# Optimization experiments

Measured on AMD Instinct MI355X. Metric: run time of the kernel, lower is better.

Reference implementation:

```python
import jax, jax.numpy as jnp
import numpy as np

B, PS, H, W = 32, 1536, 32, 64
TNS = H * W                 # total_num_selects = 2048
NJ = TNS // 16              # num_joints = 128
QK = PS // 4                # q/k channels = 384
NC = 200                    # num_classes
BN_EPS = 1e-5


def setup_inputs() -> dict:
    key = jax.random.key(0)
    ks = jax.random.split(key, 8)
    s = 0.02  # small init scale for weights
    inp = {
        "x": jax.random.normal(ks[0], (B, PS, H, W), jnp.float32),
        # param_pool0: Linear(TNS -> NJ)
        "w_pool0": jax.random.normal(ks[1], (NJ, TNS), jnp.float32) * s,
        "b_pool0": jnp.zeros((NJ,), jnp.float32),
        # learnable adjacency: eye/100 + 1/100
        "adj1": jnp.eye(NJ, dtype=jnp.float32) / 100.0 + 1.0 / 100.0,
        # conv_q1 / conv_k1: Conv1d(PS -> PS//4, kernel=1)
        "w_q": jax.random.normal(ks[2], (QK, PS), jnp.float32) * s,
        "b_q": jnp.zeros((QK,), jnp.float32),
        "w_k": jax.random.normal(ks[3], (QK, PS), jnp.float32) * s,
        "b_k": jnp.zeros((QK,), jnp.float32),
        # alpha1 (torch inits to 0; we use 0.1 so attention branch has nonzero effect/grads)
        "alpha": jnp.array([0.1], jnp.float32),
        # conv1: Conv1d(PS -> PS, kernel=1)
        "w_c1": jax.random.normal(ks[4], (PS, PS), jnp.float32) * s,
        "b_c1": jnp.zeros((PS,), jnp.float32),
        # batch_norm1 affine params
        "gamma": jnp.ones((PS,), jnp.float32),
        "beta": jnp.zeros((PS,), jnp.float32),
        # param_pool1: Linear(NJ -> 1)
        "w_pool1": jax.random.normal(ks[5], (1, NJ), jnp.float32) * s,
        "b_pool1": jnp.zeros((1,), jnp.float32),
        # classifier: Linear(PS -> NC)
        "w_cls": jax.random.normal(ks[6], (NC, PS), jnp.float32) * s,
        "b_cls": jnp.zeros((NC,), jnp.float32),
    }
    return inp


def reference(x, w_pool0, b_pool0, adj1, w_q, b_q, w_k, b_k, alpha,
              w_c1, b_c1, gamma, beta, w_pool1, b_pool1, w_cls, b_cls):
    b, c = x.shape[0], x.shape[1]
    hs = x.reshape(b, c, -1)                                   # (B, PS, TNS)
    # param_pool0: pool selects down to joints
    hs = jnp.einsum('bcs,js->bcj', hs, w_pool0) + b_pool0      # (B, PS, NJ)
    # 1x1-conv q/k then mean over channel dim
    q1 = (jnp.einsum('oc,bcj->boj', w_q, hs) + b_q[:, None]).mean(axis=1)  # (B, NJ)
    k1 = (jnp.einsum('oc,bcj->boj', w_k, hs) + b_k[:, None]).mean(axis=1)  # (B, NJ)
    # outer-difference attention, tanh-bounded, blended with learnable adjacency
    A1 = adj1 + jnp.tanh(q1[:, :, None] - k1[:, None, :]) * alpha[0]       # (B, NJ, NJ)
    # conv1 (1x1) then adjacency-weighted matmul
    hs = jnp.einsum('oc,bcj->boj', w_c1, hs) + b_c1[:, None]   # (B, PS, NJ)
    hs = jnp.einsum('bcj,bjk->bck', hs, A1)                    # (B, PS, NJ)
    # BatchNorm1d over (batch, joints) per channel (training-mode batch stats)
    mean = hs.mean(axis=(0, 2))
    var = hs.var(axis=(0, 2))
    hs = (hs - mean[None, :, None]) * jax.lax.rsqrt(var + BN_EPS)[None, :, None]
    hs = gamma[None, :, None] * hs + beta[None, :, None]
    # param_pool1 (NJ -> 1), dropout is identity in eval, flatten, classify
    hs = jnp.einsum('bcj,j->bc', hs, w_pool1[0]) + b_pool1[0]  # (B, PS)
    out = hs @ w_cls.T + b_cls                                 # (B, NC)
    return out
```

## Files before the change

### kernel.cpp

```cpp
#include <hip/hip_runtime.h>
#include <hip/hip_bf16.h>

#define B_ 32
#define PS_ 1536
#define TNS_ 2048
#define NJ_ 128
#define QK_ 384
#define NC_ 200
#define BN_EPS_ 1e-5f

typedef __attribute__((ext_vector_type(8))) short short8;
typedef __attribute__((ext_vector_type(4))) float float4v;
typedef unsigned short ushort_t;

__device__ __forceinline__ unsigned short f2b(float f) {
    unsigned int u = __float_as_uint(f);
    return (unsigned short)((u + 0x7FFFu + ((u >> 16) & 1u)) >> 16);
}
__device__ __forceinline__ float b2f_lo(unsigned int u) { return __uint_as_float(u << 16); }
__device__ __forceinline__ float b2f_hi(unsigned int u) { return __uint_as_float(u & 0xffff0000u); }

__device__ __forceinline__ void mma_chunk42(const short* As, const short* Bs,
                                            int wm, int wn, int lane, float4v acc[4][2]) {
    const int m0 = wm + (lane & 15);
    const int n0 = wn + (lane & 15);
    const int quad = lane >> 4;
    #pragma unroll
    for (int kk = 0; kk < 64; kk += 32) {
        short8 a[4], b[2];
        const int kb = quad * 8 + kk;
        #pragma unroll
        for (int i = 0; i < 4; ++i) a[i] = *(const short8*)&As[(m0 + i * 16) * 72 + kb];
        #pragma unroll
        for (int j = 0; j < 2; ++j) b[j] = *(const short8*)&Bs[(n0 + j * 16) * 72 + kb];
        #pragma unroll
        for (int i = 0; i < 4; ++i)
            #pragma unroll
            for (int j = 0; j < 2; ++j)
                acc[i][j] = __builtin_amdgcn_mfma_f32_16x16x32_bf16(a[i], b[j], acc[i][j], 0, 0, 0);
    }
}

__device__ __forceinline__ void stage_f32_512(const float* __restrict__ src, size_t stride,
                                              short* dst, int tid) {
    #pragma unroll
    for (int p = 0; p < 4; ++p) {
        int r = (tid >> 4) + p * 32;
        int kq = (tid & 15) * 4;
        float4 v = *(const float4*)(src + (size_t)r * stride + kq);
        ushort4 u = { f2b(v.x), f2b(v.y), f2b(v.z), f2b(v.w) };
        *(ushort4*)&dst[r * 72 + kq] = u;
    }
}
__device__ __forceinline__ void stage_b16_512(const ushort_t* __restrict__ src, size_t stride,
                                              short* dst, int tid) {
    #pragma unroll
    for (int p = 0; p < 2; ++p) {
        int r = (tid >> 3) + p * 64;
        int kq = (tid & 7) * 8;
        uint4 v = *(const uint4*)(src + (size_t)r * stride + kq);
        *(uint4*)&dst[r * 72 + kq] = v;
    }
}

__global__ void k_prep_all(const float* __restrict__ wq, const float* __restrict__ bq,
                           const float* __restrict__ wk, const float* __restrict__ bk,
                           const float* __restrict__ wp1,
                           const float* __restrict__ w0, const float* __restrict__ wc1,
                           float* __restrict__ wqb, float* __restrict__ wkb,
                           float* __restrict__ scal,
                           float* __restrict__ bnsum, float* __restrict__ bnsq,
                           float* __restrict__ q1, float* __restrict__ k1,
                           ushort_t* __restrict__ w0b, ushort_t* __restrict__ wc1b) {
    const int blk = blockIdx.x;
    const int tid = threadIdx.x;
    if (blk < 6) {
        int c = blk * 256 + tid;
        float s = 0.f;
        for (int o = 0; o < QK_; ++o) s += wq[(size_t)o * PS_ + c];
        wqb[c] = s * (1.0f / QK_);
        bnsum[c] = 0.f; bnsq[c] = 0.f;
    } else if (blk < 12) {
        int c = (blk - 6) * 256 + tid;
        float s = 0.f;
        for (int o = 0; o < QK_; ++o) s += wk[(size_t)o * PS_ + c];
        wkb[c] = s * (1.0f / QK_);
    } else if (blk == 12) {
        __shared__ float red[256];
        float s = (tid < QK_ ? bq[tid] : 0.f) + (tid + 256 < QK_ ? bq[tid + 256] : 0.f);
        red[tid] = s; __syncthreads();
        for (int off = 128; off > 0; off >>= 1) { if (tid < off) red[tid] += red[tid + off]; __syncthreads(); }
        if (tid == 0) scal[0] = red[0] * (1.0f / QK_);
        __syncthreads();
        s = (tid < QK_ ? bk[tid] : 0.f) + (tid + 256 < QK_ ? bk[tid + 256] : 0.f);
        red[tid] = s; __syncthreads();
        for (int off = 128; off > 0; off >>= 1) { if (tid < off) red[tid] += red[tid + off]; __syncthreads(); }
        if (tid == 0) scal[1] = red[0] * (1.0f / QK_);
        __syncthreads();
        s = (tid < NJ_ ? wp1[tid] : 0.f);
        red[tid] = s; __syncthreads();
        for (int off = 128; off > 0; off >>= 1) { if (tid < off) red[tid] += red[tid + off]; __syncthreads(); }
        if (tid == 0) scal[2] = red[0];
    } else if (blk < 269) {
        int i = (blk - 13) * 256 + tid;
        float4 v = ((const float4*)w0)[i];
        ushort4 u = { f2b(v.x), f2b(v.y), f2b(v.z), f2b(v.w) };
        ((ushort4*)w0b)[i] = u;
    } else if (blk < 2573) {
        int i = (blk - 269) * 256 + tid;
        float4 v = ((const float4*)wc1)[i];
        ushort4 u = { f2b(v.x), f2b(v.y), f2b(v.z), f2b(v.w) };
        ((ushort4*)wc1b)[i] = u;
    } else {
        int i = (blk - 2573) * 256 + tid;
        if (i < 4096) q1[i] = 0.f; else k1[i - 4096] = 0.f;
    }
}

__global__ __launch_bounds__(512) void k_gemm1(const float* __restrict__ x,
        const ushort_t* __restrict__ w0b, const float* __restrict__ b0,
        const float* __restrict__ wqb, const float* __restrict__ wkb,
        ushort_t* __restrict__ hsT, float* __restrict__ q1, float* __restrict__ k1) {
    __shared__ __align__(16) short As[128 * 72];
    __shared__ __align__(16) short Bs[128 * 72];
    const int tid = threadIdx.x, lane = tid & 63, wave = tid >> 6;
    const int wm = (wave >> 2) * 64, wn = (wave & 3) * 32;
    const size_t m0r = (size_t)blockIdx.x * 128;
    float4v acc[4][2] = {};
    for (int k0 = 0; k0 < TNS_; k0 += 64) {
        stage_f32_512(x + m0r * TNS_ + k0, TNS_, As, tid);
        stage_b16_512(w0b + k0, TNS_, Bs, tid);
        __syncthreads();
        mma_chunk42(As, Bs, wm, wn, lane, acc);
        __syncthreads();
    }
    const int b = blockIdx.x / 12, cb = (blockIdx.x % 12) * 128;
    const int quad = lane >> 4, s = lane & 15;
    float sq[2] = { 0.f, 0.f }, sk[2] = { 0.f, 0.f };
    #pragma unroll
    for (int jn = 0; jn < 2; ++jn) {
        int j = wn + jn * 16 + s;
        float bj = b0[j];
        #pragma unroll
        for (int im = 0; im < 4; ++im) {
            int c = cb + wm + im * 16 + quad * 4;
            float4v v = acc[im][jn];
            unsigned short us[4];
            #pragma unroll
            for (int r = 0; r < 4; ++r) {
                us[r] = f2b(v[r] + bj);
                float vr = b2f_lo((unsigned int)us[r]);
                sq[jn] += wqb[c + r] * vr;
                sk[jn] += wkb[c + r] * vr;
            }
            ushort4 u = { us[0], us[1], us[2], us[3] };
            *(ushort4*)&hsT[((size_t)(b * NJ_ + j)) * PS_ + c] = u;
        }
    }
    #pragma unroll
    for (int jn = 0; jn < 2; ++jn) {
        sq[jn] += __shfl_xor(sq[jn], 16, 64); sq[jn] += __shfl_xor(sq[jn], 32, 64);
        sk[jn] += __shfl_xor(sk[jn], 16, 64); sk[jn] += __shfl_xor(sk[jn], 32, 64);
    }
    if (quad == 0) {
        #pragma unroll
        for (int jn = 0; jn < 2; ++jn) {
            int j = wn + jn * 16 + s;
            atomicAdd(&q1[b * NJ_ + j], sq[jn]);
            atomicAdd(&k1[b * NJ_ + j], sk[jn]);
        }
    }
}

__global__ void k_a1(const float* __restrict__ adj, const float* __restrict__ q1,
                     const float* __restrict__ k1, const float* __restrict__ alpha,
                     const float* __restrict__ scal, ushort_t* __restrict__ A1t) {
    int idx = blockIdx.x * 256 + threadIdx.x;
    int b = idx >> 14;
    int r = idx & 16383;
    int j2 = r >> 7;
    int j = r & 127;
    float dbias = scal[0] - scal[1];
    float t = tanhf(q1[b * NJ_ + j] - k1[b * NJ_ + j2] + dbias);
    A1t[idx] = f2b(adj[j * NJ_ + j2] + t * alpha[0]);
}

__global__ __launch_bounds__(512) void k_gemm23(const ushort_t* __restrict__ wc1b,
        const float* __restrict__ bc1, const ushort_t* __restrict__ hsT,
        const ushort_t* __restrict__ A1t, const float* __restrict__ wp1,
        float* __restrict__ bnsum, float* __restrict__ bnsq, float* __restrict__ dout) {
    __shared__ __align__(16) short sm[2][128 * 72];
    __shared__ float bns_s[NJ_], bnq_s[NJ_], ds_s[NJ_];
    const int tid = threadIdx.x, lane = tid & 63, wave = tid >> 6;
    const int wm = (wave >> 2) * 64, wn = (wave & 3) * 32;
    const int b = blockIdx.y, ob = blockIdx.x * 128;
    if (tid < NJ_) { bns_s[tid] = 0.f; bnq_s[tid] = 0.f; ds_s[tid] = 0.f; }
    float4v acc[4][2] = {};
    const ushort_t* Abase = wc1b + (size_t)ob * PS_;
    const ushort_t* Bbase = hsT + (size_t)b * NJ_ * PS_;
    for (int k0 = 0; k0 < PS_; k0 += 64) {
        stage_b16_512(Abase + k0, PS_, sm[0], tid);
        stage_b16_512(Bbase + k0, PS_, sm[1], tid);
        __syncthreads();
        mma_chunk42(sm[0], sm[1], wm, wn, lane, acc);
        __syncthreads();
    }
    short* C1 = &sm[0][0];
    const int quad = lane >> 4, s = lane & 15;
    #pragma unroll
    for (int im = 0; im < 4; ++im) {
        int o0l = wm + im * 16 + quad * 4;
        float bc[4] = { bc1[ob + o0l], bc1[ob + o0l + 1], bc1[ob + o0l + 2], bc1[ob + o0l + 3] };
        #pragma unroll
        for (int jn = 0; jn < 2; ++jn) {
            int j = wn + jn * 16 + s;
            float4v v = acc[im][jn];
            #pragma unroll
            for (int r = 0; r < 4; ++r)
                C1[(o0l + r) * 136 + j] = (short)f2b(v[r] + bc[r]);
        }
    }
    __syncthreads();
    float4v acc2[4][2] = {};
    const ushort_t* Ap = A1t + (size_t)b * NJ_ * NJ_;
    const int m0 = wm + s, n0 = wn + s;
    #pragma unroll
    for (int kk = 0; kk < 128; kk += 32) {
        short8 a[4], bf[2];
        const int kb = quad * 8 + kk;
        #pragma unroll
        for (int i = 0; i < 4; ++i) a[i] = *(const short8*)&C1[(m0 + i * 16) * 136 + kb];
        #pragma unroll
        for (int j = 0; j < 2; ++j) bf[j] = *(const short8*)&Ap[(size_t)(n0 + j * 16) * NJ_ + kb];
        #pragma unroll
        for (int i = 0; i < 4; ++i)
            #pragma unroll
            for (int j = 0; j < 2; ++j)
                acc2[i][j] = __builtin_amdgcn_mfma_f32_16x16x32_bf16(a[i], bf[j], acc2[i][j], 0, 0, 0);
    }
    #pragma unroll
    for (int im = 0; im < 4; ++im) {
        float s4[4] = {}, q4[4] = {}, d4[4] = {};
        #pragma unroll
        for (int jn = 0; jn < 2; ++jn) {
            int j2 = wn + jn * 16 + s;
            float w1 = wp1[j2];
            float4v v = acc2[im][jn];
            #pragma unroll
            for (int r = 0; r < 4; ++r) {
                float vr = b2f_lo((unsigned int)f2b(v[r]));
                s4[r] += vr; q4[r] += vr * vr; d4[r] += w1 * vr;
            }
        }
        #pragma unroll
        for (int m = 1; m < 16; m <<= 1)
            #pragma unroll
            for (int r = 0; r < 4; ++r) {
                s4[r] += __shfl_xor(s4[r], m, 64);
                q4[r] += __shfl_xor(q4[r], m, 64);
                d4[r] += __shfl_xor(d4[r], m, 64);
            }
        if (s == 0) {
            #pragma unroll
            for (int r = 0; r < 4; ++r) {
                int cl = wm + im * 16 + quad * 4 + r;
                atomicAdd(&bns_s[cl], s4[r]);
                atomicAdd(&bnq_s[cl], q4[r]);
                atomicAdd(&ds_s[cl], d4[r]);
            }
        }
    }
    __syncthreads();
    if (tid < NJ_) {
        atomicAdd(&bnsum[ob + tid], bns_s[tid]);
        atomicAdd(&bnsq[ob + tid], bnq_s[tid]);
        dout[(size_t)b * PS_ + ob + tid] = ds_s[tid];
    }
}

__global__ void k_cls(const float* __restrict__ dout, const float* __restrict__ bnsum,
                      const float* __restrict__ bnsq, const float* __restrict__ gamma,
                      const float* __restrict__ beta, const float* __restrict__ scal,
                      const float* __restrict__ bp1, const float* __restrict__ wcls,
                      const float* __restrict__ bcls, float* __restrict__ out) {
    int gid = blockIdx.x * 256 + threadIdx.x;
    int w = gid >> 6;
    int lane = gid & 63;
    int b = w / 200, n = w % 200;
    const float* dp = dout + (size_t)b * PS_;
    const float* wp = wcls + (size_t)n * PS_;
    float sc2 = scal[2], bb = bp1[0];
    float acc = 0.f;
    for (int c = lane; c < PS_; c += 64) {
        float mean = bnsum[c] * (1.0f / 4096.0f);
        float var = bnsq[c] * (1.0f / 4096.0f) - mean * mean;
        float sc = gamma[c] * rsqrtf(var + BN_EPS_);
        float pval = sc * dp[c] + (beta[c] - sc * mean) * sc2 + bb;
        acc += wp[c] * pval;
    }
    #pragma unroll
    for (int off = 32; off > 0; off >>= 1) acc += __shfl_down(acc, off, 64);
    if (lane == 0) out[w] = acc + bcls[n];
}

extern "C" void kernel_launch(void* const* d_in, const int* in_sizes, int n_in,
                              void* d_out, int out_size, void* d_ws, size_t ws_size,
                              hipStream_t stream) {
    const float* x       = (const float*)d_in[0];
    const float* w_pool0 = (const float*)d_in[1];
    const float* b_pool0 = (const float*)d_in[2];
    const float* adj1    = (const float*)d_in[3];
    const float* w_q     = (const float*)d_in[4];
    const float* b_q     = (const float*)d_in[5];
    const float* w_k     = (const float*)d_in[6];
    const float* b_k     = (const float*)d_in[7];
    const float* alpha   = (const float*)d_in[8];
    const float* w_c1    = (const float*)d_in[9];
    const float* b_c1    = (const float*)d_in[10];
    const float* gamma   = (const float*)d_in[11];
    const float* beta    = (const float*)d_in[12];
    const float* w_pool1 = (const float*)d_in[13];
    const float* b_pool1 = (const float*)d_in[14];
    const float* w_cls   = (const float*)d_in[15];
    const float* b_cls   = (const float*)d_in[16];
    float* out = (float*)d_out;

    ushort_t* hsT  = (ushort_t*)d_ws;
    ushort_t* hs2  = hsT + 6291456;
    ushort_t* hs3b = hs2 + 6291456;
    ushort_t* w0b  = hs3b + 6291456;
    ushort_t* wc1b = w0b + 262144;
    ushort_t* A1t  = wc1b + 2359296;
    float* fb    = (float*)(A1t + 524288);
    float* wqb   = fb;
    float* wkb   = wqb + 1536;
    float* scal  = wkb + 1536;
    float* q1    = scal + 16;
    float* k1    = q1 + 4096;
    float* bnsum = k1 + 4096;
    float* bnsq  = bnsum + 1536;
    float* dbuf  = bnsq + 1536;
    size_t need = 44040192u + (size_t)(1536 + 1536 + 16 + 4096 + 4096 + 1536 + 1536 + 49152) * 4;
    if (ws_size < need) return;

    k_prep_all<<<2605, 256, 0, stream>>>(w_q, b_q, w_k, b_k, w_pool1, w_pool0, w_c1,
                                         wqb, wkb, scal, bnsum, bnsq, q1, k1, w0b, wc1b);
    k_gemm1 <<<384, 512, 0, stream>>>(x, w0b, b_pool0, wqb, wkb, hsT, q1, k1);
    k_a1    <<<2048, 256, 0, stream>>>(adj1, q1, k1, alpha, scal, A1t);
    k_gemm23<<<dim3(12, 32), 512, 0, stream>>>(wc1b, b_c1, hsT, A1t, w_pool1,
                                               bnsum, bnsq, dbuf);
    k_cls   <<<1600, 256, 0, stream>>>(dbuf, bnsum, bnsq, gamma, beta, scal,
                                       b_pool1, w_cls, b_cls, out);
}
```

Measured before the change: 667.8 us.

## Halve GEMM block tiles to 64 rows and swizzle gemm23 block order

Both MFMA GEMM kernels move from 128x128 tiles with 512 threads to 64x128 tiles with 256 threads. This doubles the grid to 768 blocks so the 256 CUs are better filled than with 384 blocks. k_gemm23 also flattens its grid and swizzles block indices so that blocks sharing the same batch's hsT slice are spread across the eight interleave groups. The cost is that each B tile is reloaded twice as often, and the per-block BN and dout reductions now cover 64 channels instead of 128.

```diff
diff --git a/kernel.cpp b/kernel.cpp
--- a/kernel.cpp
+++ b/kernel.cpp
@@ -21,8 +21,8 @@
 __device__ __forceinline__ float b2f_hi(unsigned int u) { return __uint_as_float(u & 0xffff0000u); }
 
 __device__ __forceinline__ void mma_chunk42(const short* As, const short* Bs,
-                                            int wm, int wn, int lane, float4v acc[4][2]) {
-    const int m0 = wm + (lane & 15);
+                                            int wn, int lane, float4v acc[4][2]) {
+    const int m0 = lane & 15;
     const int n0 = wn + (lane & 15);
     const int quad = lane >> 4;
     #pragma unroll
@@ -41,22 +41,32 @@
     }
 }
 
-__device__ __forceinline__ void stage_f32_512(const float* __restrict__ src, size_t stride,
+__device__ __forceinline__ void stage_f32_64r(const float* __restrict__ src, size_t stride,
                                               short* dst, int tid) {
     #pragma unroll
     for (int p = 0; p < 4; ++p) {
-        int r = (tid >> 4) + p * 32;
+        int r = (tid >> 4) + p * 16;
         int kq = (tid & 15) * 4;
         float4 v = *(const float4*)(src + (size_t)r * stride + kq);
         ushort4 u = { f2b(v.x), f2b(v.y), f2b(v.z), f2b(v.w) };
         *(ushort4*)&dst[r * 72 + kq] = u;
     }
 }
-__device__ __forceinline__ void stage_b16_512(const ushort_t* __restrict__ src, size_t stride,
+__device__ __forceinline__ void stage_b16_128r(const ushort_t* __restrict__ src, size_t stride,
+                                               short* dst, int tid) {
+    #pragma unroll
+    for (int p = 0; p < 4; ++p) {
+        int r = (tid >> 3) + p * 32;
+        int kq = (tid & 7) * 8;
+        uint4 v = *(const uint4*)(src + (size_t)r * stride + kq);
+        *(uint4*)&dst[r * 72 + kq] = v;
+    }
+}
+__device__ __forceinline__ void stage_b16_64r(const ushort_t* __restrict__ src, size_t stride,
                                               short* dst, int tid) {
     #pragma unroll
     for (int p = 0; p < 2; ++p) {
-        int r = (tid >> 3) + p * 64;
+        int r = (tid >> 3) + p * 32;
         int kq = (tid & 7) * 8;
         uint4 v = *(const uint4*)(src + (size_t)r * stride + kq);
         *(uint4*)&dst[r * 72 + kq] = v;
@@ -117,24 +127,25 @@
     }
 }
 
-__global__ __launch_bounds__(512) void k_gemm1(const float* __restrict__ x,
+__global__ __launch_bounds__(256) void k_gemm1(const float* __restrict__ x,
         const ushort_t* __restrict__ w0b, const float* __restrict__ b0,
         const float* __restrict__ wqb, const float* __restrict__ wkb,
         ushort_t* __restrict__ hsT, float* __restrict__ q1, float* __restrict__ k1) {
-    __shared__ __align__(16) short As[128 * 72];
-    __shared__ __align__(16) short Bs[128 * 72];
+    __shared__ __align__(16) short smem[64 * 72 + 128 * 72];
+    short* As = smem;
+    short* Bs = smem + 64 * 72;
     const int tid = threadIdx.x, lane = tid & 63, wave = tid >> 6;
-    const int wm = (wave >> 2) * 64, wn = (wave & 3) * 32;
-    const size_t m0r = (size_t)blockIdx.x * 128;
+    const int wn = wave * 32;
+    const size_t m0r = (size_t)blockIdx.x * 64;
     float4v acc[4][2] = {};
     for (int k0 = 0; k0 < TNS_; k0 += 64) {
-        stage_f32_512(x + m0r * TNS_ + k0, TNS_, As, tid);
-        stage_b16_512(w0b + k0, TNS_, Bs, tid);
-        __syncthreads();
-        mma_chunk42(As, Bs, wm, wn, lane, acc);
-        __syncthreads();
-    }
-    const int b = blockIdx.x / 12, cb = (blockIdx.x % 12) * 128;
+        stage_f32_64r(x + m0r * TNS_ + k0, TNS_, As, tid);
+        stage_b16_128r(w0b + k0, TNS_, Bs, tid);
+        __syncthreads();
+        mma_chunk42(As, Bs, wn, lane, acc);
+        __syncthreads();
+    }
+    const int b = blockIdx.x / 24, cb = (blockIdx.x % 24) * 64;
     const int quad = lane >> 4, s = lane & 15;
     float sq[2] = { 0.f, 0.f }, sk[2] = { 0.f, 0.f };
     #pragma unroll
@@ -143,7 +154,7 @@
         float bj = b0[j];
         #pragma unroll
         for (int im = 0; im < 4; ++im) {
-            int c = cb + wm + im * 16 + quad * 4;
+            int c = cb + im * 16 + quad * 4;
             float4v v = acc[im][jn];
             unsigned short us[4];
             #pragma unroll
@@ -185,31 +196,36 @@
     A1t[idx] = f2b(adj[j * NJ_ + j2] + t * alpha[0]);
 }
 
-__global__ __launch_bounds__(512) void k_gemm23(const ushort_t* __restrict__ wc1b,
+__global__ __launch_bounds__(256) void k_gemm23(const ushort_t* __restrict__ wc1b,
         const float* __restrict__ bc1, const ushort_t* __restrict__ hsT,
         const ushort_t* __restrict__ A1t, const float* __restrict__ wp1,
         float* __restrict__ bnsum, float* __restrict__ bnsq, float* __restrict__ dout) {
-    __shared__ __align__(16) short sm[2][128 * 72];
-    __shared__ float bns_s[NJ_], bnq_s[NJ_], ds_s[NJ_];
+    __shared__ __align__(16) short smem[64 * 72 + 128 * 72];
+    __shared__ float bns_s[64], bnq_s[64], ds_s[64];
+    short* As = smem;
+    short* Bs = smem + 64 * 72;
     const int tid = threadIdx.x, lane = tid & 63, wave = tid >> 6;
-    const int wm = (wave >> 2) * 64, wn = (wave & 3) * 32;
-    const int b = blockIdx.y, ob = blockIdx.x * 128;
-    if (tid < NJ_) { bns_s[tid] = 0.f; bnq_s[tid] = 0.f; ds_s[tid] = 0.f; }
+    const int wn = wave * 32;
+    const int bid = blockIdx.x;
+    const int swz = (bid & 7) * 96 + (bid >> 3);
+    const int bx = swz % 24, b = swz / 24;
+    const int ob = bx * 64;
+    if (tid < 64) { bns_s[tid] = 0.f; bnq_s[tid] = 0.f; ds_s[tid] = 0.f; }
     float4v acc[4][2] = {};
     const ushort_t* Abase = wc1b + (size_t)ob * PS_;
     const ushort_t* Bbase = hsT + (size_t)b * NJ_ * PS_;
     for (int k0 = 0; k0 < PS_; k0 += 64) {
-        stage_b16_512(Abase + k0, PS_, sm[0], tid);
-        stage_b16_512(Bbase + k0, PS_, sm[1], tid);
-        __syncthreads();
-        mma_chunk42(sm[0], sm[1], wm, wn, lane, acc);
-        __syncthreads();
-    }
-    short* C1 = &sm[0][0];
+        stage_b16_64r(Abase + k0, PS_, As, tid);
+        stage_b16_128r(Bbase + k0, PS_, Bs, tid);
+        __syncthreads();
+        mma_chunk42(As, Bs, wn, lane, acc);
+        __syncthreads();
+    }
+    short* C1 = smem;
     const int quad = lane >> 4, s = lane & 15;
     #pragma unroll
     for (int im = 0; im < 4; ++im) {
-        int o0l = wm + im * 16 + quad * 4;
+        int o0l = im * 16 + quad * 4;
         float bc[4] = { bc1[ob + o0l], bc1[ob + o0l + 1], bc1[ob + o0l + 2], bc1[ob + o0l + 3] };
         #pragma unroll
         for (int jn = 0; jn < 2; ++jn) {
@@ -223,7 +239,7 @@
     __syncthreads();
     float4v acc2[4][2] = {};
     const ushort_t* Ap = A1t + (size_t)b * NJ_ * NJ_;
-    const int m0 = wm + s, n0 = wn + s;
+    const int m0 = s, n0 = wn + s;
     #pragma unroll
     for (int kk = 0; kk < 128; kk += 32) {
         short8 a[4], bf[2];
@@ -263,7 +279,7 @@
         if (s == 0) {
             #pragma unroll
             for (int r = 0; r < 4; ++r) {
-                int cl = wm + im * 16 + quad * 4 + r;
+                int cl = im * 16 + quad * 4 + r;
                 atomicAdd(&bns_s[cl], s4[r]);
                 atomicAdd(&bnq_s[cl], q4[r]);
                 atomicAdd(&ds_s[cl], d4[r]);
@@ -271,7 +287,7 @@
         }
     }
     __syncthreads();
-    if (tid < NJ_) {
+    if (tid < 64) {
         atomicAdd(&bnsum[ob + tid], bns_s[tid]);
         atomicAdd(&bnsq[ob + tid], bnq_s[tid]);
         dout[(size_t)b * PS_ + ob + tid] = ds_s[tid];
@@ -345,10 +361,10 @@
 
     k_prep_all<<<2605, 256, 0, stream>>>(w_q, b_q, w_k, b_k, w_pool1, w_pool0, w_c1,
                                          wqb, wkb, scal, bnsum, bnsq, q1, k1, w0b, wc1b);
-    k_gemm1 <<<384, 512, 0, stream>>>(x, w0b, b_pool0, wqb, wkb, hsT, q1, k1);
+    k_gemm1 <<<768, 256, 0, stream>>>(x, w0b, b_pool0, wqb, wkb, hsT, q1, k1);
     k_a1    <<<2048, 256, 0, stream>>>(adj1, q1, k1, alpha, scal, A1t);
-    k_gemm23<<<dim3(12, 32), 512, 0, stream>>>(wc1b, b_c1, hsT, A1t, w_pool1,
-                                               bnsum, bnsq, dbuf);
+    k_gemm23<<<768, 256, 0, stream>>>(wc1b, b_c1, hsT, A1t, w_pool1,
+                                      bnsum, bnsq, dbuf);
     k_cls   <<<1600, 256, 0, stream>>>(dbuf, bnsum, bnsq, gamma, beta, scal,
                                        b_pool1, w_cls, b_cls, out);
 }
```

Measured after the change: 684.9 us. +2.6%, slower.
